# Optimization experiments

Hardware: AMD Instinct MI355X
Metric: run time of the kernel (lower is better)

The kernel has to match this reference:

```python
import jax, jax.numpy as jnp
import numpy as np

N = 20000        # nodes
E = 320000       # edges (before self-loops)
G = 128          # graphs
NODE_DIM = 128
H = 256
L = 4
EPS = 1e-5


def setup_inputs() -> dict:
    key = jax.random.key(0)
    ks = jax.random.split(key, 12)
    x = jax.random.normal(ks[0], (N, NODE_DIM), jnp.float32)
    edge_index = jax.random.randint(ks[1], (2, E), 0, N, dtype=jnp.int32)
    batch = jnp.sort(jax.random.randint(ks[2], (N,), 0, G, dtype=jnp.int32))
    s_in = 1.0 / np.sqrt(NODE_DIM)
    s_h = 1.0 / np.sqrt(H)
    return {
        "x": x,
        "edge_index": edge_index,
        "batch": batch,
        "enc_w": jax.random.normal(ks[3], (NODE_DIM, H), jnp.float32) * s_in,
        "enc_b": jnp.zeros((H,), jnp.float32),
        "conv_w": jax.random.normal(ks[4], (L, H, H), jnp.float32) * s_h,
        "conv_b": jnp.zeros((L, H), jnp.float32),
        "bn_gamma": jnp.ones((L, H), jnp.float32),
        "bn_beta": jnp.zeros((L, H), jnp.float32),
        "bn_mean": jnp.zeros((L, H), jnp.float32),
        "bn_var": jnp.ones((L, H), jnp.float32),
        "head_w1": jax.random.normal(ks[5], (2 * H, H), jnp.float32) * (1.0 / np.sqrt(2 * H)),
        "head_b1": jnp.zeros((H,), jnp.float32),
        "head_w2": jax.random.normal(ks[6], (H, 1), jnp.float32) * s_h,
        "head_b2": jnp.zeros((1,), jnp.float32),
    }


def reference(x, edge_index, batch, enc_w, enc_b, conv_w, conv_b,
              bn_gamma, bn_beta, bn_mean, bn_var,
              head_w1, head_b1, head_w2, head_b2):
    seg = jax.ops.segment_sum
    # GCN normalization with added self-loops (PyG GCNConv default)
    loops = jnp.arange(N, dtype=edge_index.dtype)
    src = jnp.concatenate([edge_index[0], loops])
    dst = jnp.concatenate([edge_index[1], loops])
    deg = seg(jnp.ones(src.shape[0], x.dtype), dst, num_segments=N)  # >= 1
    dinv = jax.lax.rsqrt(deg)
    norm = dinv[src] * dinv[dst]  # [E+N]

    h = x @ enc_w + enc_b  # [N, H]
    for l in range(L):
        m = h @ conv_w[l]                                    # transform
        m = seg(m[src] * norm[:, None], dst, num_segments=N)  # gather-norm-scatter
        m = m + conv_b[l]
        m = jax.nn.relu(m)
        # BatchNorm1d (eval mode: running stats); dropout inactive in eval
        m = (m - bn_mean[l]) * jax.lax.rsqrt(bn_var[l] + EPS) * bn_gamma[l] + bn_beta[l]
        h = h + m  # residual

    # global mean + add pooling over graphs
    sums = seg(h, batch, num_segments=G)                     # [G, H]
    counts = seg(jnp.ones((N,), h.dtype), batch, num_segments=G)
    mean = sums / jnp.maximum(counts, 1.0)[:, None]
    g = jnp.concatenate([mean, sums], axis=-1)               # [G, 2H]

    out = jax.nn.relu(g @ head_w1 + head_b1) @ head_w2 + head_b2
    return out.squeeze(-1)  # [G]
```

## Files before the change

### kernel.cpp

```cpp
#include <hip/hip_runtime.h>

#define N_NODES 20000
#define N_EDGES 320000
#define N_GRAPHS 128
#define IN_DIM 128
#define HDIM 256
#define LAYERS 4
#define EPSV 1e-5f
#define PCH 16
#define ELLS 64
#define NBLK_AGG (N_NODES / 4)

#define XQ (N_NODES * IN_DIM / 4)
#define ENC_N (HDIM * IN_DIM)
#define CONV_N (LAYERS * HDIM * HDIM)
#define BN_N (LAYERS * HDIM)
#define PREP_TOTAL (XQ + ENC_N + CONV_N + BN_N + N_NODES)

typedef unsigned short u16;
typedef unsigned char u8;
typedef __attribute__((ext_vector_type(8))) __bf16 bf16x8;
typedef __attribute__((ext_vector_type(4))) float f32x4;
typedef __attribute__((ext_vector_type(2))) float f32x2;
typedef __attribute__((ext_vector_type(8))) unsigned short u16x8;

__device__ __forceinline__ u16 f2bf(float f) {
    unsigned int u = __float_as_uint(f);
    u += 0x7FFFu + ((u >> 16) & 1u);
    return (u16)(u >> 16);
}
__device__ __forceinline__ float bf2f(u16 s) {
    return __uint_as_float((unsigned int)s << 16);
}
__device__ __forceinline__ u8 f2fp8(float v) {
    return (u8)(__builtin_amdgcn_cvt_pk_fp8_f32(v, v, 0, false) & 0xff);
}
__device__ __forceinline__ void fp8x8_to_f32(uint2 v, float* o) {
    f32x2 a0 = __builtin_amdgcn_cvt_pk_f32_fp8(v.x, false);
    f32x2 a1 = __builtin_amdgcn_cvt_pk_f32_fp8(v.x, true);
    f32x2 a2 = __builtin_amdgcn_cvt_pk_f32_fp8(v.y, false);
    f32x2 a3 = __builtin_amdgcn_cvt_pk_f32_fp8(v.y, true);
    o[0] = a0.x; o[1] = a0.y; o[2] = a1.x; o[3] = a1.y;
    o[4] = a2.x; o[5] = a2.y; o[6] = a3.x; o[7] = a3.y;
}

__global__ __launch_bounds__(256) void k_prep(
    const float* __restrict__ x, u16* __restrict__ xb,
    const float* __restrict__ enc_w, u16* __restrict__ encT,
    const float* __restrict__ conv_w, u16* __restrict__ convT,
    const float* __restrict__ gamma, const float* __restrict__ beta,
    const float* __restrict__ mean, const float* __restrict__ var,
    float* __restrict__ bnA, float* __restrict__ bnB, int* __restrict__ cnt)
{
    int idx = blockIdx.x * 256 + threadIdx.x;
    if (idx < XQ) {
        float4 v = *reinterpret_cast<const float4*>(x + (size_t)idx * 4);
        ushort4 o;
        o.x = f2bf(v.x); o.y = f2bf(v.y); o.z = f2bf(v.z); o.w = f2bf(v.w);
        *reinterpret_cast<ushort4*>(xb + (size_t)idx * 4) = o;
        return;
    }
    idx -= XQ;
    if (idx < ENC_N) {
        int n = idx / IN_DIM, k = idx - n * IN_DIM;
        encT[idx] = f2bf(enc_w[(size_t)k * HDIM + n]);
        return;
    }
    idx -= ENC_N;
    if (idx < CONV_N) {
        int l = idx >> 16, i = idx & 65535;
        int n = i >> 8, k = i & 255;
        convT[idx] = f2bf(conv_w[((size_t)l << 16) + (size_t)k * HDIM + n]);
        return;
    }
    idx -= CONV_N;
    if (idx < BN_N) {
        float A = gamma[idx] * rsqrtf(var[idx] + EPSV);
        bnA[idx] = A;
        bnB[idx] = beta[idx] - mean[idx] * A;
        return;
    }
    idx -= BN_N;
    if (idx < N_NODES) cnt[idx] = 0;
}

__global__ void k_scatter_ell(const int* __restrict__ src, const int* __restrict__ dst,
                              int* __restrict__ cnt, int* __restrict__ col) {
    int e = blockIdx.x * 256 + threadIdx.x;
    if (e < N_EDGES) {
        int d = dst[e];
        int s = src[e];
        int p = atomicAdd(&cnt[d], 1);
        if (p < ELLS) col[(size_t)d * ELLS + p] = s;
    }
}

__device__ __forceinline__ bf16x8 load_frag(const u16* __restrict__ lds, int r, int g) {
    const char* rb = (const char*)(lds + r * 32);
    int s = (r & 3) << 4;
    union { struct { unsigned long long lo, hi; } q; bf16x8 v; } u;
    u.q.lo = *(const unsigned long long*)(rb + ((g * 8) ^ s));
    u.q.hi = *(const unsigned long long*)(rb + ((32 + g * 8) ^ s));
    return u.v;
}

template <int K, int MODE>
__global__ __launch_bounds__(256) void k_gemm_mfma(
    const u16* __restrict__ A, const u16* __restrict__ BT,
    const float* __restrict__ bias, u16* __restrict__ Cb,
    u8* __restrict__ Cf8, int M)
{
    constexpr int NT2 = K / 64;
    __shared__ u16 As[2][2][128 * 32];
    __shared__ u16 Bs[2][2][64 * 32];
    const int tid = threadIdx.x;
    const int lane = tid & 63;
    const int wr = tid >> 6;
    const int m0 = blockIdx.x * 128, n0 = blockIdx.y * 64;
    const int g = lane >> 4, lr = lane & 15;

    f32x4 acc[2][4] = {};

    auto stage = [&](int buf, int k0) {
        #pragma unroll
        for (int kk = 0; kk < 2; kk++) {
            #pragma unroll
            for (int j = 0; j < 2; j++) {
                int q = tid + 256 * j;
                int r = q >> 2, c4 = q & 3;
                int boff = (c4 * 16) ^ ((r & 3) << 4);
                int arow = m0 + r; if (arow >= M) arow = M - 1;
                const char* ga = (const char*)(A + (size_t)arow * K + k0 + kk * 32) + boff;
                __builtin_amdgcn_global_load_lds(
                    (const __attribute__((address_space(1))) void*)ga,
                    (__attribute__((address_space(3))) void*)((char*)As[buf][kk] + q * 16),
                    16, 0, 0);
            }
            {
                int q = tid;
                int r = q >> 2, c4 = q & 3;
                int boff = (c4 * 16) ^ ((r & 3) << 4);
                const char* gb = (const char*)(BT + (size_t)(n0 + r) * K + k0 + kk * 32) + boff;
                __builtin_amdgcn_global_load_lds(
                    (const __attribute__((address_space(1))) void*)gb,
                    (__attribute__((address_space(3))) void*)((char*)Bs[buf][kk] + q * 16),
                    16, 0, 0);
            }
        }
    };

    stage(0, 0);
    #pragma unroll
    for (int kt = 0; kt < NT2; kt++) {
        const int cur = kt & 1;
        if (kt + 1 < NT2) {
            stage(cur ^ 1, (kt + 1) * 64);
            asm volatile("s_waitcnt vmcnt(6)" ::: "memory");
        } else {
            asm volatile("s_waitcnt vmcnt(0)" ::: "memory");
        }
        __builtin_amdgcn_sched_barrier(0);
        __builtin_amdgcn_s_barrier();
        __builtin_amdgcn_sched_barrier(0);

        #pragma unroll
        for (int kk = 0; kk < 2; kk++) {
            bf16x8 af[2], bfr[4];
            #pragma unroll
            for (int mi = 0; mi < 2; mi++)
                af[mi] = load_frag(As[cur][kk], wr * 32 + mi * 16 + lr, g);
            #pragma unroll
            for (int ni = 0; ni < 4; ni++)
                bfr[ni] = load_frag(Bs[cur][kk], ni * 16 + lr, g);
            #pragma unroll
            for (int mi = 0; mi < 2; mi++)
                #pragma unroll
                for (int ni = 0; ni < 4; ni++)
                    acc[mi][ni] = __builtin_amdgcn_mfma_f32_16x16x32_bf16(
                        af[mi], bfr[ni], acc[mi][ni], 0, 0, 0);
        }

        asm volatile("s_waitcnt lgkmcnt(0)" ::: "memory");
        __builtin_amdgcn_sched_barrier(0);
        __builtin_amdgcn_s_barrier();
        __builtin_amdgcn_sched_barrier(0);
    }

    #pragma unroll
    for (int mi = 0; mi < 2; mi++) {
        #pragma unroll
        for (int rg = 0; rg < 4; rg++) {
            int row = m0 + wr * 32 + mi * 16 + g * 4 + rg;
            if (row >= M) continue;
            #pragma unroll
            for (int ni = 0; ni < 4; ni++) {
                int colg = n0 + ni * 16 + lr;
                float v = acc[mi][ni][rg];
                if (MODE == 0) {
                    v += bias[colg];
                    Cb[(size_t)row * HDIM + colg] = f2bf(v);
                } else {
                    Cf8[(size_t)row * HDIM + colg] = f2fp8(v);
                }
            }
        }
    }
}

__global__ __launch_bounds__(256) void k_aggregate(
    const u8* __restrict__ mf8, const int* __restrict__ cnt,
    const int* __restrict__ col,
    const float* __restrict__ cb, const float* __restrict__ bnA,
    const float* __restrict__ bnB, u16* __restrict__ hb)
{
    const int node = blockIdx.x * 4 + (threadIdx.x >> 6);
    const int lane = threadIdx.x & 63;
    const int p = lane >> 5;
    const int c = (lane & 31) * 8;
    int nb = cnt[node]; if (nb > ELLS) nb = ELLS;
    const float di = rsqrtf((float)nb + 1.0f);

    int s_l = 0; float w_l = 0.f;
    if (lane < nb) {
        s_l = col[(size_t)node * ELLS + lane];
        w_l = rsqrtf((float)cnt[s_l] + 1.0f) * di;
    }

    float a[8] = {};
    if (p == 0) {
        float dii = di * di;
        uint2 v = *reinterpret_cast<const uint2*>(mf8 + (size_t)node * HDIM + c);
        float f[8]; fp8x8_to_f32(v, f);
        #pragma unroll
        for (int j = 0; j < 8; j++) a[j] = dii * f[j];
    }

    const int iters = (nb + 1) >> 1;
    for (int t = 0; t < iters; t += 8) {
        int e = 2 * t + p;
        int   s0 = __shfl(s_l, e,      64); float w0 = __shfl(w_l, e,      64);
        int   s1 = __shfl(s_l, e + 2,  64); float w1 = __shfl(w_l, e + 2,  64);
        int   s2 = __shfl(s_l, e + 4,  64); float w2 = __shfl(w_l, e + 4,  64);
        int   s3 = __shfl(s_l, e + 6,  64); float w3 = __shfl(w_l, e + 6,  64);
        int   s4 = __shfl(s_l, e + 8,  64); float w4 = __shfl(w_l, e + 8,  64);
        int   s5 = __shfl(s_l, e + 10, 64); float w5 = __shfl(w_l, e + 10, 64);
        int   s6 = __shfl(s_l, e + 12, 64); float w6 = __shfl(w_l, e + 12, 64);
        int   s7 = __shfl(s_l, e + 14, 64); float w7 = __shfl(w_l, e + 14, 64);
        uint2 v0 = *reinterpret_cast<const uint2*>(mf8 + (size_t)s0 * HDIM + c);
        uint2 v1 = *reinterpret_cast<const uint2*>(mf8 + (size_t)s1 * HDIM + c);
        uint2 v2 = *reinterpret_cast<const uint2*>(mf8 + (size_t)s2 * HDIM + c);
        uint2 v3 = *reinterpret_cast<const uint2*>(mf8 + (size_t)s3 * HDIM + c);
        uint2 v4 = *reinterpret_cast<const uint2*>(mf8 + (size_t)s4 * HDIM + c);
        uint2 v5 = *reinterpret_cast<const uint2*>(mf8 + (size_t)s5 * HDIM + c);
        uint2 v6 = *reinterpret_cast<const uint2*>(mf8 + (size_t)s6 * HDIM + c);
        uint2 v7 = *reinterpret_cast<const uint2*>(mf8 + (size_t)s7 * HDIM + c);
        float f0[8], f1[8], f2[8], f3[8], f4[8], f5[8], f6[8], f7[8];
        fp8x8_to_f32(v0, f0); fp8x8_to_f32(v1, f1);
        fp8x8_to_f32(v2, f2); fp8x8_to_f32(v3, f3);
        fp8x8_to_f32(v4, f4); fp8x8_to_f32(v5, f5);
        fp8x8_to_f32(v6, f6); fp8x8_to_f32(v7, f7);
        #pragma unroll
        for (int j = 0; j < 8; j++) {
            a[j] += w0 * f0[j] + w1 * f1[j];
            a[j] += w2 * f2[j] + w3 * f3[j];
            a[j] += w4 * f4[j] + w5 * f5[j];
            a[j] += w6 * f6[j] + w7 * f7[j];
        }
    }

    #pragma unroll
    for (int j = 0; j < 8; j++) a[j] += __shfl_xor(a[j], 32, 64);

    if (p == 0) {
        const size_t base = (size_t)node * HDIM + c;
        u16x8 rv = *reinterpret_cast<const u16x8*>(hb + base);
        float4 cb0 = *reinterpret_cast<const float4*>(cb + c);
        float4 cb1 = *reinterpret_cast<const float4*>(cb + c + 4);
        float4 A0 = *reinterpret_cast<const float4*>(bnA + c);
        float4 A1 = *reinterpret_cast<const float4*>(bnA + c + 4);
        float4 B0 = *reinterpret_cast<const float4*>(bnB + c);
        float4 B1 = *reinterpret_cast<const float4*>(bnB + c + 4);
        float cbv[8] = {cb0.x, cb0.y, cb0.z, cb0.w, cb1.x, cb1.y, cb1.z, cb1.w};
        float Av[8] = {A0.x, A0.y, A0.z, A0.w, A1.x, A1.y, A1.z, A1.w};
        float Bv[8] = {B0.x, B0.y, B0.z, B0.w, B1.x, B1.y, B1.z, B1.w};
        u16x8 hbv;
        #pragma unroll
        for (int j = 0; j < 8; j++) {
            float v = fmaxf(a[j] + cbv[j], 0.f);
            hbv[j] = f2bf(bf2f(rv[j]) + v * Av[j] + Bv[j]);
        }
        *reinterpret_cast<u16x8*>(hb + base) = hbv;
    }
}

__device__ __forceinline__ int lower_bound_dev(const int* a, int n, int key) {
    int lo = 0, hi = n;
    while (lo < hi) {
        int mid = (lo + hi) >> 1;
        if (a[mid] < key) lo = mid + 1; else hi = mid;
    }
    return lo;
}

__global__ __launch_bounds__(256) void k_pool_partial(const u16* __restrict__ hb,
                                                      const int* __restrict__ batch,
                                                      float* __restrict__ pbuf) {
    int g = blockIdx.x / PCH, c = blockIdx.x % PCH;
    int t = threadIdx.x;
    int start = lower_bound_dev(batch, N_NODES, g);
    int end = lower_bound_dev(batch, N_NODES, g + 1);
    int len = end - start;
    int s0 = start + (int)(((long long)len * c) / PCH);
    int s1 = start + (int)(((long long)len * (c + 1)) / PCH);
    float acc = 0.f;
    for (int n = s0; n < s1; n++) acc += bf2f(hb[(size_t)n * HDIM + t]);
    pbuf[(size_t)blockIdx.x * HDIM + t] = acc;
}

__global__ __launch_bounds__(256) void k_head(const float* __restrict__ pbuf,
                                              const int* __restrict__ batch,
                                              const float* __restrict__ w1,
                                              const float* __restrict__ b1,
                                              const float* __restrict__ w2,
                                              const float* __restrict__ b2,
                                              float* __restrict__ out) {
    int g = blockIdx.x;
    int t = threadIdx.x;
    __shared__ float gs[512];
    __shared__ float red[256];
    float s = 0.f;
    #pragma unroll
    for (int c = 0; c < PCH; c++) s += pbuf[(size_t)(g * PCH + c) * HDIM + t];
    int start = lower_bound_dev(batch, N_NODES, g);
    int end = lower_bound_dev(batch, N_NODES, g + 1);
    float cntf = fmaxf((float)(end - start), 1.0f);
    gs[t] = s / cntf;
    gs[256 + t] = s;
    __syncthreads();
    float acc = b1[t];
    for (int k = 0; k < 512; k++) acc += gs[k] * w1[(size_t)k * HDIM + t];
    acc = fmaxf(acc, 0.f);
    red[t] = acc * w2[t];
    __syncthreads();
    for (int s2 = 128; s2 > 0; s2 >>= 1) {
        if (t < s2) red[t] += red[t + s2];
        __syncthreads();
    }
    if (t == 0) out[g] = red[0] + b2[0];
}

extern "C" void kernel_launch(void* const* d_in, const int* in_sizes, int n_in,
                              void* d_out, int out_size, void* d_ws, size_t ws_size,
                              hipStream_t stream) {
    const float* x      = (const float*)d_in[0];
    const int*   ei     = (const int*)d_in[1];
    const int*   srcIdx = ei;
    const int*   dstIdx = ei + N_EDGES;
    const int*   batch  = (const int*)d_in[2];
    const float* enc_w  = (const float*)d_in[3];
    const float* enc_b  = (const float*)d_in[4];
    const float* conv_w = (const float*)d_in[5];
    const float* conv_b = (const float*)d_in[6];
    const float* gamma  = (const float*)d_in[7];
    const float* beta   = (const float*)d_in[8];
    const float* bmean  = (const float*)d_in[9];
    const float* bvar   = (const float*)d_in[10];
    const float* w1     = (const float*)d_in[11];
    const float* b1     = (const float*)d_in[12];
    const float* w2     = (const float*)d_in[13];
    const float* b2     = (const float*)d_in[14];
    float* out = (float*)d_out;

    char* ws = (char*)d_ws;
    size_t off = 0;
    auto alloc = [&](size_t bytes) -> void* {
        void* p = ws + off;
        off = (off + bytes + 255) & ~(size_t)255;
        return p;
    };
    int*   cnt    = (int*)alloc((size_t)N_NODES * 4);
    int*   col    = (int*)alloc((size_t)N_NODES * ELLS * 4);
    u16*   hb     = (u16*)alloc((size_t)N_NODES * HDIM * 2);
    u8*    mf8    = (u8*)alloc((size_t)N_NODES * HDIM * 1);
    u16*   encT   = (u16*)alloc((size_t)HDIM * IN_DIM * 2);
    u16*   convT  = (u16*)alloc((size_t)LAYERS * HDIM * HDIM * 2);
    float* bnA    = (float*)alloc((size_t)LAYERS * HDIM * 4);
    float* bnB    = (float*)alloc((size_t)LAYERS * HDIM * 4);
    float* pbuf   = (float*)alloc((size_t)N_GRAPHS * PCH * HDIM * 4);
    u16*   xb     = (u16*)mf8;

    const int nb_edges = (N_EDGES + 255) / 256;

    k_prep<<<(PREP_TOTAL + 255) / 256, 256, 0, stream>>>(
        x, xb, enc_w, encT, conv_w, convT, gamma, beta, bmean, bvar, bnA, bnB, cnt);

    k_scatter_ell<<<nb_edges, 256, 0, stream>>>(srcIdx, dstIdx, cnt, col);

    dim3 gg((N_NODES + 127) / 128, HDIM / 64);
    k_gemm_mfma<IN_DIM, 0><<<gg, 256, 0, stream>>>(xb, encT, enc_b, hb, nullptr, N_NODES);

    for (int l = 0; l < LAYERS; l++) {
        k_gemm_mfma<HDIM, 1><<<gg, 256, 0, stream>>>(
            hb, convT + (size_t)l * HDIM * HDIM, nullptr, nullptr, mf8, N_NODES);
        k_aggregate<<<NBLK_AGG, 256, 0, stream>>>(
            mf8, cnt, col,
            conv_b + (size_t)l * HDIM, bnA + (size_t)l * HDIM, bnB + (size_t)l * HDIM,
            hb);
    }

    k_pool_partial<<<N_GRAPHS * PCH, 256, 0, stream>>>(hb, batch, pbuf);
    k_head<<<N_GRAPHS, 256, 0, stream>>>(pbuf, batch, w1, b1, w2, b2, out);
}
```

Before: 200.2 us.

## Deepen GEMM pipeline, tile weight transpose via LDS, shrink ELL indices to u16

The GEMM moves from a two-buffer pipeline over 64-wide K steps to a four-buffer ring of 32-wide K stages with two stages in flight, which drops the trailing barrier on each iteration. The weight transpose in the prep kernel now goes through 64x64 LDS tiles so that reads and writes are both coalesced. ELL column indices are stored as u16, which halves the index traffic in scatter and aggregate. The index narrowing relies on N_NODES fitting in 16 bits, and removing the second barrier depends on the 4-slot ring keeping the buffer being overwritten separate from the one being read.

Result: no change. 201.8 us, median of 2 (+0.8%).

```diff
diff --git a/kernel.cpp b/kernel.cpp
--- a/kernel.cpp
+++ b/kernel.cpp
@@ -10,12 +10,11 @@
 #define PCH 16
 #define ELLS 64
 #define NBLK_AGG (N_NODES / 4)
+#define WTILES 72
 
 #define XQ (N_NODES * IN_DIM / 4)
-#define ENC_N (HDIM * IN_DIM)
-#define CONV_N (LAYERS * HDIM * HDIM)
 #define BN_N (LAYERS * HDIM)
-#define PREP_TOTAL (XQ + ENC_N + CONV_N + BN_N + N_NODES)
+#define ELEM_TOTAL (XQ + BN_N + N_NODES)
 
 typedef unsigned short u16;
 typedef unsigned char u8;
@@ -52,7 +51,39 @@
     const float* __restrict__ mean, const float* __restrict__ var,
     float* __restrict__ bnA, float* __restrict__ bnB, int* __restrict__ cnt)
 {
-    int idx = blockIdx.x * 256 + threadIdx.x;
+    __shared__ u16 tile[64][65];
+    const int tid = threadIdx.x;
+    if (blockIdx.x < WTILES) {
+        int w = blockIdx.x;
+        const float* src; u16* dst; int k0, n0, ncols, kdim;
+        if (w < 8) {
+            int kt = w >> 2, nt = w & 3;
+            k0 = kt * 64; n0 = nt * 64; ncols = HDIM; kdim = IN_DIM;
+            src = enc_w; dst = encT;
+        } else {
+            w -= 8;
+            int l = w >> 4, t = w & 15;
+            int kt = t >> 2, nt = t & 3;
+            k0 = kt * 64; n0 = nt * 64; ncols = HDIM; kdim = HDIM;
+            src = conv_w + (size_t)l * HDIM * HDIM;
+            dst = convT + (size_t)l * HDIM * HDIM;
+        }
+        #pragma unroll
+        for (int pass = 0; pass < 16; pass++) {
+            int idx = pass * 256 + tid;
+            int r = idx >> 6, c = idx & 63;
+            tile[r][c] = f2bf(src[(size_t)(k0 + r) * ncols + n0 + c]);
+        }
+        __syncthreads();
+        #pragma unroll
+        for (int pass = 0; pass < 16; pass++) {
+            int idx = pass * 256 + tid;
+            int rn = idx >> 6, ck = idx & 63;
+            dst[(size_t)(n0 + rn) * kdim + k0 + ck] = tile[ck][rn];
+        }
+        return;
+    }
+    int idx = (blockIdx.x - WTILES) * 256 + tid;
     if (idx < XQ) {
         float4 v = *reinterpret_cast<const float4*>(x + (size_t)idx * 4);
         ushort4 o;
@@ -61,19 +92,6 @@
         return;
     }
     idx -= XQ;
-    if (idx < ENC_N) {
-        int n = idx / IN_DIM, k = idx - n * IN_DIM;
-        encT[idx] = f2bf(enc_w[(size_t)k * HDIM + n]);
-        return;
-    }
-    idx -= ENC_N;
-    if (idx < CONV_N) {
-        int l = idx >> 16, i = idx & 65535;
-        int n = i >> 8, k = i & 255;
-        convT[idx] = f2bf(conv_w[((size_t)l << 16) + (size_t)k * HDIM + n]);
-        return;
-    }
-    idx -= CONV_N;
     if (idx < BN_N) {
         float A = gamma[idx] * rsqrtf(var[idx] + EPSV);
         bnA[idx] = A;
@@ -85,13 +103,13 @@
 }
 
 __global__ void k_scatter_ell(const int* __restrict__ src, const int* __restrict__ dst,
-                              int* __restrict__ cnt, int* __restrict__ col) {
+                              int* __restrict__ cnt, u16* __restrict__ col) {
     int e = blockIdx.x * 256 + threadIdx.x;
     if (e < N_EDGES) {
         int d = dst[e];
         int s = src[e];
         int p = atomicAdd(&cnt[d], 1);
-        if (p < ELLS) col[(size_t)d * ELLS + p] = s;
+        if (p < ELLS) col[(size_t)d * ELLS + p] = (u16)s;
     }
 }
 
@@ -110,9 +128,9 @@
     const float* __restrict__ bias, u16* __restrict__ Cb,
     u8* __restrict__ Cf8, int M)
 {
-    constexpr int NT2 = K / 64;
-    __shared__ u16 As[2][2][128 * 32];
-    __shared__ u16 Bs[2][2][64 * 32];
+    constexpr int NT = K / 32;
+    __shared__ u16 As[4][128 * 32];
+    __shared__ u16 Bs[4][64 * 32];
     const int tid = threadIdx.x;
     const int lane = tid & 63;
     const int wr = tid >> 6;
@@ -123,39 +141,36 @@
 
     auto stage = [&](int buf, int k0) {
         #pragma unroll
-        for (int kk = 0; kk < 2; kk++) {
-            #pragma unroll
-            for (int j = 0; j < 2; j++) {
-                int q = tid + 256 * j;
-                int r = q >> 2, c4 = q & 3;
-                int boff = (c4 * 16) ^ ((r & 3) << 4);
-                int arow = m0 + r; if (arow >= M) arow = M - 1;
-                const char* ga = (const char*)(A + (size_t)arow * K + k0 + kk * 32) + boff;
-                __builtin_amdgcn_global_load_lds(
-                    (const __attribute__((address_space(1))) void*)ga,
-                    (__attribute__((address_space(3))) void*)((char*)As[buf][kk] + q * 16),
-                    16, 0, 0);
-            }
-            {
-                int q = tid;
-                int r = q >> 2, c4 = q & 3;
-                int boff = (c4 * 16) ^ ((r & 3) << 4);
-                const char* gb = (const char*)(BT + (size_t)(n0 + r) * K + k0 + kk * 32) + boff;
-                __builtin_amdgcn_global_load_lds(
-                    (const __attribute__((address_space(1))) void*)gb,
-                    (__attribute__((address_space(3))) void*)((char*)Bs[buf][kk] + q * 16),
-                    16, 0, 0);
-            }
+        for (int j = 0; j < 2; j++) {
+            int q = tid + 256 * j;
+            int r = q >> 2, c4 = q & 3;
+            int boff = (c4 * 16) ^ ((r & 3) << 4);
+            int arow = m0 + r; if (arow >= M) arow = M - 1;
+            const char* ga = (const char*)(A + (size_t)arow * K + k0) + boff;
+            __builtin_amdgcn_global_load_lds(
+                (const __attribute__((address_space(1))) void*)ga,
+                (__attribute__((address_space(3))) void*)((char*)As[buf] + q * 16), 16, 0, 0);
+        }
+        {
+            int q = tid;
+            int r = q >> 2, c4 = q & 3;
+            int boff = (c4 * 16) ^ ((r & 3) << 4);
+            const char* gb = (const char*)(BT + (size_t)(n0 + r) * K + k0) + boff;
+            __builtin_amdgcn_global_load_lds(
+                (const __attribute__((address_space(1))) void*)gb,
+                (__attribute__((address_space(3))) void*)((char*)Bs[buf] + q * 16), 16, 0, 0);
         }
     };
 
     stage(0, 0);
+    stage(1, 32);
     #pragma unroll
-    for (int kt = 0; kt < NT2; kt++) {
-        const int cur = kt & 1;
-        if (kt + 1 < NT2) {
-            stage(cur ^ 1, (kt + 1) * 64);
+    for (int kt = 0; kt < NT; kt++) {
+        if (kt + 2 < NT) {
+            stage((kt + 2) & 3, (kt + 2) * 32);
             asm volatile("s_waitcnt vmcnt(6)" ::: "memory");
+        } else if (kt + 1 < NT) {
+            asm volatile("s_waitcnt vmcnt(3)" ::: "memory");
         } else {
             asm volatile("s_waitcnt vmcnt(0)" ::: "memory");
         }
@@ -163,27 +178,20 @@
         __builtin_amdgcn_s_barrier();
         __builtin_amdgcn_sched_barrier(0);
 
-        #pragma unroll
-        for (int kk = 0; kk < 2; kk++) {
-            bf16x8 af[2], bfr[4];
-            #pragma unroll
-            for (int mi = 0; mi < 2; mi++)
-                af[mi] = load_frag(As[cur][kk], wr * 32 + mi * 16 + lr, g);
+        const int cur = kt & 3;
+        bf16x8 af[2], bfr[4];
+        #pragma unroll
+        for (int mi = 0; mi < 2; mi++)
+            af[mi] = load_frag(As[cur], wr * 32 + mi * 16 + lr, g);
+        #pragma unroll
+        for (int ni = 0; ni < 4; ni++)
+            bfr[ni] = load_frag(Bs[cur], ni * 16 + lr, g);
+        #pragma unroll
+        for (int mi = 0; mi < 2; mi++)
             #pragma unroll
             for (int ni = 0; ni < 4; ni++)
-                bfr[ni] = load_frag(Bs[cur][kk], ni * 16 + lr, g);
-            #pragma unroll
-            for (int mi = 0; mi < 2; mi++)
-                #pragma unroll
-                for (int ni = 0; ni < 4; ni++)
-                    acc[mi][ni] = __builtin_amdgcn_mfma_f32_16x16x32_bf16(
-                        af[mi], bfr[ni], acc[mi][ni], 0, 0, 0);
-        }
-
-        asm volatile("s_waitcnt lgkmcnt(0)" ::: "memory");
-        __builtin_amdgcn_sched_barrier(0);
-        __builtin_amdgcn_s_barrier();
-        __builtin_amdgcn_sched_barrier(0);
+                acc[mi][ni] = __builtin_amdgcn_mfma_f32_16x16x32_bf16(
+                    af[mi], bfr[ni], acc[mi][ni], 0, 0, 0);
     }
 
     #pragma unroll
@@ -209,7 +217,7 @@
 
 __global__ __launch_bounds__(256) void k_aggregate(
     const u8* __restrict__ mf8, const int* __restrict__ cnt,
-    const int* __restrict__ col,
+    const u16* __restrict__ col,
     const float* __restrict__ cb, const float* __restrict__ bnA,
     const float* __restrict__ bnB, u16* __restrict__ hb)
 {
@@ -222,7 +230,7 @@
 
     int s_l = 0; float w_l = 0.f;
     if (lane < nb) {
-        s_l = col[(size_t)node * ELLS + lane];
+        s_l = (int)col[(size_t)node * ELLS + lane];
         w_l = rsqrtf((float)cnt[s_l] + 1.0f) * di;
     }
 
@@ -379,7 +387,7 @@
         return p;
     };
     int*   cnt    = (int*)alloc((size_t)N_NODES * 4);
-    int*   col    = (int*)alloc((size_t)N_NODES * ELLS * 4);
+    u16*   col    = (u16*)alloc((size_t)N_NODES * ELLS * 2);
     u16*   hb     = (u16*)alloc((size_t)N_NODES * HDIM * 2);
     u8*    mf8    = (u8*)alloc((size_t)N_NODES * HDIM * 1);
     u16*   encT   = (u16*)alloc((size_t)HDIM * IN_DIM * 2);
@@ -391,7 +399,7 @@
 
     const int nb_edges = (N_EDGES + 255) / 256;
 
-    k_prep<<<(PREP_TOTAL + 255) / 256, 256, 0, stream>>>(
+    k_prep<<<WTILES + (ELEM_TOTAL + 255) / 256, 256, 0, stream>>>(
         x, xb, enc_w, encT, conv_w, convT, gamma, beta, bmean, bvar, bnA, bnB, cnt);
 
     k_scatter_ell<<<nb_edges, 256, 0, stream>>>(srcIdx, dstIdx, cnt, col);
```
